# Kernel tuning notes

Hardware: AMD Instinct MI355X
Metric: run time of the kernel (lower is better)

Reference implementation:

```python
import jax, jax.numpy as jnp
import numpy as np

HEADS = 4
HEAD_DIM = 32
IN_DIM = 128
N_TRIG = 48
N_SPAN = 128


def build_edges(T, S):
    # nodes are (trig r, span c) flattened row-major: n = r*S + c
    N = T * S
    nodes = jnp.arange(N, dtype=jnp.int32)
    r = nodes // S
    c = nodes % S
    # same-row neighbors (includes self loop once): [N, S]
    row_nb = r[:, None] * S + jnp.arange(S, dtype=jnp.int32)[None, :]
    # same-column neighbors excluding own row: [N, T-1]
    t_idx = jnp.arange(T - 1, dtype=jnp.int32)[None, :]
    t = t_idx + (t_idx >= r[:, None]).astype(jnp.int32)
    col_nb = t * S + c[:, None]
    deg = S + T - 1
    src = jnp.concatenate([row_nb, col_nb], axis=1).reshape(-1)  # [N*deg]
    dst = jnp.repeat(nodes, deg)
    return src, dst, N


def gat_conv(x, src, dst, N, W, att_src, att_dst, bias):
    # PyG GATConv (eval mode, dropout off), concat=True.
    # W: [in, H*Hd]; att_src/att_dst: [H, Hd]; bias: [H*Hd]
    h = (x @ W).reshape(N, HEADS, HEAD_DIM)          # [N,H,Hd]
    a_src = jnp.sum(h * att_src[None], axis=-1)      # [N,H]
    a_dst = jnp.sum(h * att_dst[None], axis=-1)      # [N,H]
    e = jax.nn.leaky_relu(a_src[src] + a_dst[dst], negative_slope=0.2)  # [E,H]
    # scatter-softmax over incoming edges per destination node
    m = jax.ops.segment_max(e, dst, num_segments=N)  # [N,H]
    ex = jnp.exp(e - m[dst])
    denom = jax.ops.segment_sum(ex, dst, num_segments=N)
    alpha = ex / denom[dst]                          # [E,H]
    msg = alpha[:, :, None] * h[src]                 # [E,H,Hd]
    out = jax.ops.segment_sum(msg, dst, num_segments=N)  # [N,H,Hd]
    return out.reshape(N, HEADS * HEAD_DIM) + bias[None]


def setup_inputs() -> dict:
    key = jax.random.key(0)
    ks = jax.random.split(key, 9)
    D = IN_DIM
    HD = HEADS * HEAD_DIM
    inp = {
        "pair_embeddings": jax.random.normal(ks[0], (1, N_TRIG, N_SPAN, D), dtype=jnp.float32),
        "W1": jax.random.normal(ks[1], (D, HD), dtype=jnp.float32) * (2.0 / (D + HD)) ** 0.5,
        "att_src1": jax.random.normal(ks[2], (HEADS, HEAD_DIM), dtype=jnp.float32) * 0.1,
        "att_dst1": jax.random.normal(ks[3], (HEADS, HEAD_DIM), dtype=jnp.float32) * 0.1,
        "b1": jnp.zeros((HD,), dtype=jnp.float32),
        "W2": jax.random.normal(ks[4], (HD, HD), dtype=jnp.float32) * (2.0 / (HD + HD)) ** 0.5,
        "att_src2": jax.random.normal(ks[5], (HEADS, HEAD_DIM), dtype=jnp.float32) * 0.1,
        "att_dst2": jax.random.normal(ks[6], (HEADS, HEAD_DIM), dtype=jnp.float32) * 0.1,
        "b2": jnp.zeros((HD,), dtype=jnp.float32),
        "num_trigs_kept": N_TRIG,
        "num_arg_spans_kept": N_SPAN,
    }
    return inp


def reference(pair_embeddings, W1, att_src1, att_dst1, b1, W2, att_src2, att_dst2, b2, num_trigs_kept, num_arg_spans_kept):
    T, S = int(num_trigs_kept), int(num_arg_spans_kept)
    src, dst, N = build_edges(T, S)
    # batch_size == 1: slice and flatten node features
    x = pair_embeddings[0, :T, :S].reshape(N, -1)
    x = jax.nn.elu(gat_conv(x, src, dst, N, W1, att_src1, att_dst1, b1))
    x = jax.nn.elu(gat_conv(x, src, dst, N, W2, att_src2, att_dst2, b2))
    return x
```

## Files before the change

kernel.cpp:

```cpp
#include <hip/hip_runtime.h>

#define T_TRIG 48
#define S_SPAN 128
#define NN (T_TRIG * S_SPAN)
#define D 128

typedef __attribute__((ext_vector_type(8))) short sh8;
typedef __attribute__((ext_vector_type(4))) float f32x4;

__device__ inline unsigned short f2bf(float v) {
    unsigned u = __float_as_uint(v);
    unsigned r = u + 0x7FFFu + ((u >> 16) & 1u);
    return (unsigned short)(r >> 16);
}
__device__ inline float bf2f(unsigned short b) {
    return __uint_as_float(((unsigned)b) << 16);
}

__global__ __launch_bounds__(64) void pack_w_kernel(
    const float* __restrict__ W1, const float* __restrict__ W2,
    unsigned short* __restrict__ w1h, unsigned short* __restrict__ w1l,
    unsigned short* __restrict__ w2h, unsigned short* __restrict__ w2l)
{
    const int b = blockIdx.x;
    const int l = threadIdx.x;
    const float* W = (b < 8) ? W1 : W2;
    unsigned short* wh = (b < 8) ? w1h : w2h;
    unsigned short* wl = (b < 8) ? w1l : w2l;
    const int nt = b & 7;
    const int n = nt * 16 + (l & 15);
    const int kgb = (l >> 4) * 8;

    #pragma unroll
    for (int kc = 0; kc < 4; ++kc) {
        unsigned short hb[8], lb[8];
        #pragma unroll
        for (int i = 0; i < 8; ++i) {
            int k = kc * 32 + kgb + i;
            float v = W[k * D + n];
            unsigned short h = f2bf(v);
            hb[i] = h;
            lb[i] = f2bf(v - bf2f(h));
        }
        size_t base = ((size_t)(nt * 4 + kc) * 64 + l) * 8;
        #pragma unroll
        for (int i = 0; i < 8; ++i) { wh[base + i] = hb[i]; wl[base + i] = lb[i]; }
    }
}

__global__ __launch_bounds__(64) void gemm_mfma_kernel(
    const float* __restrict__ X,
    const unsigned short* __restrict__ Wh, const unsigned short* __restrict__ Wl,
    const float* __restrict__ att_s, const float* __restrict__ att_d,
    float* __restrict__ H, float* __restrict__ asrc, float* __restrict__ adst)
{
    const int l = threadIdx.x;
    const int mt = blockIdx.x >> 1;
    const int nh = blockIdx.x & 1;
    const int c = l & 15;
    const int kg = l >> 4;
    const int row0 = mt * 16;

    const sh8* Wh8 = (const sh8*)Wh;
    const sh8* Wl8 = (const sh8*)Wl;

    f32x4 acc[4] = {f32x4{0,0,0,0}, f32x4{0,0,0,0}, f32x4{0,0,0,0}, f32x4{0,0,0,0}};

    #pragma unroll
    for (int kc = 0; kc < 4; ++kc) {
        const float* xp = X + (size_t)(row0 + c) * D + kc * 32 + kg * 8;
        float4 x0 = *(const float4*)xp;
        float4 x1 = *(const float4*)(xp + 4);
        float xs[8] = {x0.x, x0.y, x0.z, x0.w, x1.x, x1.y, x1.z, x1.w};
        sh8 ah, al;
        #pragma unroll
        for (int i = 0; i < 8; ++i) {
            unsigned short h = f2bf(xs[i]);
            ah[i] = (short)h;
            al[i] = (short)f2bf(xs[i] - bf2f(h));
        }
        #pragma unroll
        for (int ntl = 0; ntl < 4; ++ntl) {
            int ntg = nh * 4 + ntl;
            sh8 bh = Wh8[(ntg * 4 + kc) * 64 + l];
            sh8 bl = Wl8[(ntg * 4 + kc) * 64 + l];
            acc[ntl] = __builtin_amdgcn_mfma_f32_16x16x32_bf16(ah, bh, acc[ntl], 0, 0, 0);
            acc[ntl] = __builtin_amdgcn_mfma_f32_16x16x32_bf16(al, bh, acc[ntl], 0, 0, 0);
            acc[ntl] = __builtin_amdgcn_mfma_f32_16x16x32_bf16(ah, bl, acc[ntl], 0, 0, 0);
        }
    }

    #pragma unroll
    for (int ntl = 0; ntl < 4; ++ntl) {
        #pragma unroll
        for (int i = 0; i < 4; ++i) {
            H[(size_t)(row0 + kg * 4 + i) * D + nh * 64 + ntl * 16 + c] = acc[ntl][i];
        }
    }

    float asv[4], adv[4];
    #pragma unroll
    for (int ntl = 0; ntl < 4; ++ntl) {
        int d = (nh * 2 + (ntl >> 1)) * 32 + (ntl & 1) * 16 + c;
        asv[ntl] = att_s[d];
        adv[ntl] = att_d[d];
    }
    #pragma unroll
    for (int i = 0; i < 4; ++i) {
        float ps0 = acc[0][i] * asv[0] + acc[1][i] * asv[1];
        float ps1 = acc[2][i] * asv[2] + acc[3][i] * asv[3];
        float pd0 = acc[0][i] * adv[0] + acc[1][i] * adv[1];
        float pd1 = acc[2][i] * adv[2] + acc[3][i] * adv[3];
        #pragma unroll
        for (int o = 1; o < 16; o <<= 1) {
            ps0 += __shfl_xor(ps0, o); ps1 += __shfl_xor(ps1, o);
            pd0 += __shfl_xor(pd0, o); pd1 += __shfl_xor(pd1, o);
        }
        if (c == 0) {
            int rr = row0 + kg * 4 + i;
            asrc[rr * 4 + nh * 2 + 0] = ps0;
            asrc[rr * 4 + nh * 2 + 1] = ps1;
            adst[rr * 4 + nh * 2 + 0] = pd0;
            adst[rr * 4 + nh * 2 + 1] = pd1;
        }
    }
}

__global__ __launch_bounds__(256) void row_agg_kernel(
    const float* __restrict__ H, const float* __restrict__ asrc,
    const float* __restrict__ adst, float* __restrict__ num_row,
    float* __restrict__ den_row)
{
    __shared__ float sh_h[S_SPAN][32];
    __shared__ float sh_as[S_SPAN];
    const int tid = threadIdx.x;
    const int r = blockIdx.x >> 2;
    const int h = blockIdx.x & 3;
    const int base = r * S_SPAN;

    #pragma unroll
    for (int it = 0; it < 4; ++it) {
        int chunk = tid + it * 256;
        int cp = chunk >> 3, fc = chunk & 7;
        *(float4*)&sh_h[cp][fc * 4] =
            *(const float4*)&H[(size_t)(base + cp) * D + h * 32 + fc * 4];
    }
    if (tid < S_SPAN) sh_as[tid] = asrc[(base + tid) * 4 + h];
    __syncthreads();

    const int fg = tid & 3;
    const int cth = tid >> 2;
    const float ad0 = adst[(base + cth) * 4 + h];
    const float ad1 = adst[(base + cth + 64) * 4 + h];
    float4 n00 = {0,0,0,0}, n01 = {0,0,0,0}, n10 = {0,0,0,0}, n11 = {0,0,0,0};
    float den0 = 0.f, den1 = 0.f;

    #pragma unroll 2
    for (int cp = 0; cp < S_SPAN; ++cp) {
        float a = sh_as[cp];
        float4 h0 = *(float4*)&sh_h[cp][fg * 8];
        float4 h1 = *(float4*)&sh_h[cp][fg * 8 + 4];
        float e0 = a + ad0; e0 = fmaxf(e0, 0.2f * e0);
        float e1 = a + ad1; e1 = fmaxf(e1, 0.2f * e1);
        float w0 = __expf(e0);
        float w1 = __expf(e1);
        den0 += w0; den1 += w1;
        n00.x = fmaf(w0, h0.x, n00.x); n00.y = fmaf(w0, h0.y, n00.y);
        n00.z = fmaf(w0, h0.z, n00.z); n00.w = fmaf(w0, h0.w, n00.w);
        n01.x = fmaf(w0, h1.x, n01.x); n01.y = fmaf(w0, h1.y, n01.y);
        n01.z = fmaf(w0, h1.z, n01.z); n01.w = fmaf(w0, h1.w, n01.w);
        n10.x = fmaf(w1, h0.x, n10.x); n10.y = fmaf(w1, h0.y, n10.y);
        n10.z = fmaf(w1, h0.z, n10.z); n10.w = fmaf(w1, h0.w, n10.w);
        n11.x = fmaf(w1, h1.x, n11.x); n11.y = fmaf(w1, h1.y, n11.y);
        n11.z = fmaf(w1, h1.z, n11.z); n11.w = fmaf(w1, h1.w, n11.w);
    }

    const int n0 = base + cth, n1 = n0 + 64;
    *(float4*)&num_row[(size_t)n0 * D + h * 32 + fg * 8]     = n00;
    *(float4*)&num_row[(size_t)n0 * D + h * 32 + fg * 8 + 4] = n01;
    *(float4*)&num_row[(size_t)n1 * D + h * 32 + fg * 8]     = n10;
    *(float4*)&num_row[(size_t)n1 * D + h * 32 + fg * 8 + 4] = n11;
    if (fg == 0) {
        den_row[n0 * 4 + h] = den0;
        den_row[n1 * 4 + h] = den1;
    }
}

__global__ __launch_bounds__(256) void col_agg_kernel(
    const float* __restrict__ H, const float* __restrict__ asrc,
    const float* __restrict__ adst, const float* __restrict__ num_row,
    const float* __restrict__ den_row, const float* __restrict__ bias,
    float* __restrict__ out)
{
    __shared__ float sh_h[T_TRIG][D];
    __shared__ float sh_as[4][T_TRIG];
    const int c = blockIdx.x;
    const int tid = threadIdx.x;

    #pragma unroll
    for (int it = 0; it < 6; ++it) {
        int chunk = tid + it * 256;
        int t = chunk >> 5, fc = chunk & 31;
        *(float4*)&sh_h[t][fc * 4] =
            *(const float4*)&H[(size_t)(t * S_SPAN + c) * D + fc * 4];
    }
    if (tid < 4 * T_TRIG) {
        int hh = tid / T_TRIG, t = tid - hh * T_TRIG;
        sh_as[hh][t] = asrc[(t * S_SPAN + c) * 4 + hh];
    }
    __syncthreads();

    const int f4g = tid & 31;
    const int tg = tid >> 5;
    const int head = f4g >> 3;

    float4 num[6];
    float den[6], ad[6];
    #pragma unroll
    for (int dd = 0; dd < 6; ++dd) {
        num[dd] = {0,0,0,0};
        den[dd] = 0.f;
        ad[dd] = adst[((tg * 6 + dd) * S_SPAN + c) * 4 + head];
    }

    for (int tp = 0; tp < T_TRIG; ++tp) {
        float a = sh_as[head][tp];
        float4 hv = *(float4*)&sh_h[tp][f4g * 4];
        #pragma unroll
        for (int dd = 0; dd < 6; ++dd) {
            float e = a + ad[dd];
            e = fmaxf(e, 0.2f * e);
            float w = __expf(e);
            w = (tp == tg * 6 + dd) ? 0.f : w;
            den[dd] += w;
            num[dd].x = fmaf(w, hv.x, num[dd].x);
            num[dd].y = fmaf(w, hv.y, num[dd].y);
            num[dd].z = fmaf(w, hv.z, num[dd].z);
            num[dd].w = fmaf(w, hv.w, num[dd].w);
        }
    }

    const float4 b4 = *(const float4*)&bias[f4g * 4];
    #pragma unroll
    for (int dd = 0; dd < 6; ++dd) {
        int n = (tg * 6 + dd) * S_SPAN + c;
        float4 nr = *(const float4*)&num_row[(size_t)n * D + f4g * 4];
        float dr = den_row[n * 4 + head];
        float inv = 1.f / (dr + den[dd]);
        float4 o;
        o.x = (nr.x + num[dd].x) * inv + b4.x;
        o.y = (nr.y + num[dd].y) * inv + b4.y;
        o.z = (nr.z + num[dd].z) * inv + b4.z;
        o.w = (nr.w + num[dd].w) * inv + b4.w;
        o.x = o.x > 0.f ? o.x : (__expf(o.x) - 1.f);
        o.y = o.y > 0.f ? o.y : (__expf(o.y) - 1.f);
        o.z = o.z > 0.f ? o.z : (__expf(o.z) - 1.f);
        o.w = o.w > 0.f ? o.w : (__expf(o.w) - 1.f);
        *(float4*)&out[(size_t)n * D + f4g * 4] = o;
    }
}

extern "C" void kernel_launch(void* const* d_in, const int* in_sizes, int n_in,
                              void* d_out, int out_size, void* d_ws, size_t ws_size,
                              hipStream_t stream)
{
    const float* pe  = (const float*)d_in[0];
    const float* W1  = (const float*)d_in[1];
    const float* as1 = (const float*)d_in[2];
    const float* ad1 = (const float*)d_in[3];
    const float* b1  = (const float*)d_in[4];
    const float* W2  = (const float*)d_in[5];
    const float* as2 = (const float*)d_in[6];
    const float* ad2 = (const float*)d_in[7];
    const float* b2  = (const float*)d_in[8];
    float* out = (float*)d_out;

    char* ws = (char*)d_ws;
    float* H     = (float*)ws;
    float* X2    = H + (size_t)NN * D;
    float* numr  = X2 + (size_t)NN * D;
    float* asrcb = numr + (size_t)NN * D;
    float* adstb = asrcb + (size_t)NN * 4;
    float* denb  = adstb + (size_t)NN * 4;
    unsigned short* w1h = (unsigned short*)(denb + (size_t)NN * 4);
    unsigned short* w1l = w1h + 128 * 128;
    unsigned short* w2h = w1l + 128 * 128;
    unsigned short* w2l = w2h + 128 * 128;

    pack_w_kernel<<<dim3(16), dim3(64), 0, stream>>>(W1, W2, w1h, w1l, w2h, w2l);

    gemm_mfma_kernel<<<dim3(768), dim3(64), 0, stream>>>(pe, w1h, w1l, as1, ad1, H, asrcb, adstb);
    row_agg_kernel<<<dim3(T_TRIG * 4), dim3(256), 0, stream>>>(H, asrcb, adstb, numr, denb);
    col_agg_kernel<<<dim3(S_SPAN), dim3(256), 0, stream>>>(H, asrcb, adstb, numr, denb, b1, X2);
    gemm_mfma_kernel<<<dim3(768), dim3(64), 0, stream>>>(X2, w2h, w2l, as2, ad2, H, asrcb, adstb);
    row_agg_kernel<<<dim3(T_TRIG * 4), dim3(256), 0, stream>>>(H, asrcb, adstb, numr, denb);
    col_agg_kernel<<<dim3(S_SPAN), dim3(256), 0, stream>>>(H, asrcb, adstb, numr, denb, b2, out);
}
```

Measured before the change: 78.42 us.

## Pre-split activations into bf16 hi/lo and widen GEMM to 4 waves per block

Input activations are now converted to bf16 hi/lo pairs once, in a prep kernel for layer 1 and in the col_agg epilogue for layer 2, so the GEMM loads pre-packed operands instead of converting fp32 per block. The GEMM block grows to 256 threads, with each wave owning one 16-column tile, and the attention-score reduction is finished through shared memory. The weight packing is folded into the same prep launch. The split format writes and reads two bf16 buffers in place of one fp32 buffer, and the prep pass adds extra traffic over the layer-1 input.

Result: slower. 81.57 us (+4.0%).

```diff
diff --git a/kernel.cpp b/kernel.cpp
--- a/kernel.cpp
+++ b/kernel.cpp
@@ -7,6 +7,7 @@
 
 typedef __attribute__((ext_vector_type(8))) short sh8;
 typedef __attribute__((ext_vector_type(4))) float f32x4;
+typedef __attribute__((ext_vector_type(4))) unsigned short us4;
 
 __device__ inline unsigned short f2bf(float v) {
     unsigned u = __float_as_uint(v);
@@ -17,27 +18,28 @@
     return __uint_as_float(((unsigned)b) << 16);
 }
 
-__global__ __launch_bounds__(64) void pack_w_kernel(
-    const float* __restrict__ W1, const float* __restrict__ W2,
+__global__ __launch_bounds__(256) void prep_kernel(
+    const float* __restrict__ pe, const float* __restrict__ W1,
+    const float* __restrict__ W2,
+    unsigned short* __restrict__ x1h, unsigned short* __restrict__ x1l,
     unsigned short* __restrict__ w1h, unsigned short* __restrict__ w1l,
     unsigned short* __restrict__ w2h, unsigned short* __restrict__ w2l)
 {
     const int b = blockIdx.x;
-    const int l = threadIdx.x;
-    const float* W = (b < 8) ? W1 : W2;
-    unsigned short* wh = (b < 8) ? w1h : w2h;
-    unsigned short* wl = (b < 8) ? w1l : w2l;
-    const int nt = b & 7;
-    const int n = nt * 16 + (l & 15);
-    const int kgb = (l >> 4) * 8;
-
-    #pragma unroll
-    for (int kc = 0; kc < 4; ++kc) {
+    const int t = threadIdx.x;
+    if (b < 16) {
+        const float* W = (b < 8) ? W1 : W2;
+        unsigned short* wh = (b < 8) ? w1h : w2h;
+        unsigned short* wl = (b < 8) ? w1l : w2l;
+        const int nt = b & 7;
+        const int kc = t >> 6;
+        const int l = t & 63;
+        const int n = nt * 16 + (l & 15);
+        const int kb = kc * 32 + (l >> 4) * 8;
         unsigned short hb[8], lb[8];
         #pragma unroll
         for (int i = 0; i < 8; ++i) {
-            int k = kc * 32 + kgb + i;
-            float v = W[k * D + n];
+            float v = W[(kb + i) * D + n];
             unsigned short h = f2bf(v);
             hb[i] = h;
             lb[i] = f2bf(v - bf2f(h));
@@ -45,84 +47,87 @@
         size_t base = ((size_t)(nt * 4 + kc) * 64 + l) * 8;
         #pragma unroll
         for (int i = 0; i < 8; ++i) { wh[base + i] = hb[i]; wl[base + i] = lb[i]; }
-    }
-}
-
-__global__ __launch_bounds__(64) void gemm_mfma_kernel(
-    const float* __restrict__ X,
+    } else {
+        const int idx = (b - 16) * 256 + t;
+        const float* p = pe + (size_t)idx * 8;
+        float4 v0 = *(const float4*)p;
+        float4 v1 = *(const float4*)(p + 4);
+        float xs[8] = {v0.x, v0.y, v0.z, v0.w, v1.x, v1.y, v1.z, v1.w};
+        sh8 hv, lv;
+        #pragma unroll
+        for (int i = 0; i < 8; ++i) {
+            unsigned short h = f2bf(xs[i]);
+            hv[i] = (short)h;
+            lv[i] = (short)f2bf(xs[i] - bf2f(h));
+        }
+        ((sh8*)x1h)[idx] = hv;
+        ((sh8*)x1l)[idx] = lv;
+    }
+}
+
+__global__ __launch_bounds__(256) void gemm_mfma_kernel(
+    const unsigned short* __restrict__ Xh, const unsigned short* __restrict__ Xl,
     const unsigned short* __restrict__ Wh, const unsigned short* __restrict__ Wl,
     const float* __restrict__ att_s, const float* __restrict__ att_d,
     float* __restrict__ H, float* __restrict__ asrc, float* __restrict__ adst)
 {
-    const int l = threadIdx.x;
+    __shared__ float ps_part[4][16], pd_part[4][16];
+
+    const int t = threadIdx.x;
+    const int w = t >> 6;
+    const int l = t & 63;
     const int mt = blockIdx.x >> 1;
-    const int nh = blockIdx.x & 1;
+    const int nq = blockIdx.x & 1;
+    const int nt = nq * 4 + w;
     const int c = l & 15;
     const int kg = l >> 4;
     const int row0 = mt * 16;
 
+    const sh8* Xh8 = (const sh8*)Xh;
+    const sh8* Xl8 = (const sh8*)Xl;
     const sh8* Wh8 = (const sh8*)Wh;
     const sh8* Wl8 = (const sh8*)Wl;
 
-    f32x4 acc[4] = {f32x4{0,0,0,0}, f32x4{0,0,0,0}, f32x4{0,0,0,0}, f32x4{0,0,0,0}};
-
+    f32x4 acc = {0, 0, 0, 0};
     #pragma unroll
     for (int kc = 0; kc < 4; ++kc) {
-        const float* xp = X + (size_t)(row0 + c) * D + kc * 32 + kg * 8;
-        float4 x0 = *(const float4*)xp;
-        float4 x1 = *(const float4*)(xp + 4);
-        float xs[8] = {x0.x, x0.y, x0.z, x0.w, x1.x, x1.y, x1.z, x1.w};
-        sh8 ah, al;
-        #pragma unroll
-        for (int i = 0; i < 8; ++i) {
-            unsigned short h = f2bf(xs[i]);
-            ah[i] = (short)h;
-            al[i] = (short)f2bf(xs[i] - bf2f(h));
-        }
-        #pragma unroll
-        for (int ntl = 0; ntl < 4; ++ntl) {
-            int ntg = nh * 4 + ntl;
-            sh8 bh = Wh8[(ntg * 4 + kc) * 64 + l];
-            sh8 bl = Wl8[(ntg * 4 + kc) * 64 + l];
-            acc[ntl] = __builtin_amdgcn_mfma_f32_16x16x32_bf16(ah, bh, acc[ntl], 0, 0, 0);
-            acc[ntl] = __builtin_amdgcn_mfma_f32_16x16x32_bf16(al, bh, acc[ntl], 0, 0, 0);
-            acc[ntl] = __builtin_amdgcn_mfma_f32_16x16x32_bf16(ah, bl, acc[ntl], 0, 0, 0);
-        }
-    }
-
-    #pragma unroll
-    for (int ntl = 0; ntl < 4; ++ntl) {
-        #pragma unroll
-        for (int i = 0; i < 4; ++i) {
-            H[(size_t)(row0 + kg * 4 + i) * D + nh * 64 + ntl * 16 + c] = acc[ntl][i];
-        }
-    }
-
-    float asv[4], adv[4];
-    #pragma unroll
-    for (int ntl = 0; ntl < 4; ++ntl) {
-        int d = (nh * 2 + (ntl >> 1)) * 32 + (ntl & 1) * 16 + c;
-        asv[ntl] = att_s[d];
-        adv[ntl] = att_d[d];
-    }
+        const int xi = (row0 + c) * 16 + kc * 4 + kg;
+        sh8 ah = Xh8[xi];
+        sh8 al = Xl8[xi];
+        sh8 bh = Wh8[(nt * 4 + kc) * 64 + l];
+        sh8 bl = Wl8[(nt * 4 + kc) * 64 + l];
+        acc = __builtin_amdgcn_mfma_f32_16x16x32_bf16(ah, bh, acc, 0, 0, 0);
+        acc = __builtin_amdgcn_mfma_f32_16x16x32_bf16(al, bh, acc, 0, 0, 0);
+        acc = __builtin_amdgcn_mfma_f32_16x16x32_bf16(ah, bl, acc, 0, 0, 0);
+    }
+
+    #pragma unroll
+    for (int i = 0; i < 4; ++i)
+        H[(size_t)(row0 + kg * 4 + i) * D + nt * 16 + c] = acc[i];
+
+    const int dim = (nt >> 1) * 32 + (nt & 1) * 16 + c;
+    const float asv = att_s[dim];
+    const float adv = att_d[dim];
     #pragma unroll
     for (int i = 0; i < 4; ++i) {
-        float ps0 = acc[0][i] * asv[0] + acc[1][i] * asv[1];
-        float ps1 = acc[2][i] * asv[2] + acc[3][i] * asv[3];
-        float pd0 = acc[0][i] * adv[0] + acc[1][i] * adv[1];
-        float pd1 = acc[2][i] * adv[2] + acc[3][i] * adv[3];
-        #pragma unroll
-        for (int o = 1; o < 16; o <<= 1) {
-            ps0 += __shfl_xor(ps0, o); ps1 += __shfl_xor(ps1, o);
-            pd0 += __shfl_xor(pd0, o); pd1 += __shfl_xor(pd1, o);
-        }
+        float ps = acc[i] * asv;
+        float pd = acc[i] * adv;
+        ps += __shfl_xor(ps, 1); pd += __shfl_xor(pd, 1);
+        ps += __shfl_xor(ps, 2); pd += __shfl_xor(pd, 2);
+        ps += __shfl_xor(ps, 4); pd += __shfl_xor(pd, 4);
+        ps += __shfl_xor(ps, 8); pd += __shfl_xor(pd, 8);
         if (c == 0) {
-            int rr = row0 + kg * 4 + i;
-            asrc[rr * 4 + nh * 2 + 0] = ps0;
-            asrc[rr * 4 + nh * 2 + 1] = ps1;
-            adst[rr * 4 + nh * 2 + 0] = pd0;
-            adst[rr * 4 + nh * 2 + 1] = pd1;
-        }
+            ps_part[w][kg * 4 + i] = ps;
+            pd_part[w][kg * 4 + i] = pd;
+        }
+    }
+    __syncthreads();
+    if (t < 32) {
+        const int row = t & 15;
+        const int hh = t >> 4;
+        const int head = nq * 2 + hh;
+        asrc[(row0 + row) * 4 + head] = ps_part[2 * hh][row] + ps_part[2 * hh + 1][row];
+        adst[(row0 + row) * 4 + head] = pd_part[2 * hh][row] + pd_part[2 * hh + 1][row];
     }
 }
 
@@ -190,7 +195,8 @@
     const float* __restrict__ H, const float* __restrict__ asrc,
     const float* __restrict__ adst, const float* __restrict__ num_row,
     const float* __restrict__ den_row, const float* __restrict__ bias,
-    float* __restrict__ out)
+    float* __restrict__ out, unsigned short* __restrict__ xh,
+    unsigned short* __restrict__ xl)
 {
     __shared__ float sh_h[T_TRIG][D];
     __shared__ float sh_as[4][T_TRIG];
@@ -247,16 +253,28 @@
         float4 nr = *(const float4*)&num_row[(size_t)n * D + f4g * 4];
         float dr = den_row[n * 4 + head];
         float inv = 1.f / (dr + den[dd]);
-        float4 o;
-        o.x = (nr.x + num[dd].x) * inv + b4.x;
-        o.y = (nr.y + num[dd].y) * inv + b4.y;
-        o.z = (nr.z + num[dd].z) * inv + b4.z;
-        o.w = (nr.w + num[dd].w) * inv + b4.w;
-        o.x = o.x > 0.f ? o.x : (__expf(o.x) - 1.f);
-        o.y = o.y > 0.f ? o.y : (__expf(o.y) - 1.f);
-        o.z = o.z > 0.f ? o.z : (__expf(o.z) - 1.f);
-        o.w = o.w > 0.f ? o.w : (__expf(o.w) - 1.f);
-        *(float4*)&out[(size_t)n * D + f4g * 4] = o;
+        float o[4];
+        o[0] = (nr.x + num[dd].x) * inv + b4.x;
+        o[1] = (nr.y + num[dd].y) * inv + b4.y;
+        o[2] = (nr.z + num[dd].z) * inv + b4.z;
+        o[3] = (nr.w + num[dd].w) * inv + b4.w;
+        #pragma unroll
+        for (int q = 0; q < 4; ++q)
+            o[q] = o[q] > 0.f ? o[q] : (__expf(o[q]) - 1.f);
+        if (xh) {
+            us4 hv4, lv4;
+            #pragma unroll
+            for (int q = 0; q < 4; ++q) {
+                unsigned short hq = f2bf(o[q]);
+                hv4[q] = hq;
+                lv4[q] = f2bf(o[q] - bf2f(hq));
+            }
+            *(us4*)&xh[(size_t)n * D + f4g * 4] = hv4;
+            *(us4*)&xl[(size_t)n * D + f4g * 4] = lv4;
+        } else {
+            float4 o4 = {o[0], o[1], o[2], o[3]};
+            *(float4*)&out[(size_t)n * D + f4g * 4] = o4;
+        }
     }
 }
 
@@ -277,22 +295,30 @@
 
     char* ws = (char*)d_ws;
     float* H     = (float*)ws;
-    float* X2    = H + (size_t)NN * D;
-    float* numr  = X2 + (size_t)NN * D;
+    float* numr  = H + (size_t)NN * D;
     float* asrcb = numr + (size_t)NN * D;
     float* adstb = asrcb + (size_t)NN * 4;
     float* denb  = adstb + (size_t)NN * 4;
-    unsigned short* w1h = (unsigned short*)(denb + (size_t)NN * 4);
-    unsigned short* w1l = w1h + 128 * 128;
-    unsigned short* w2h = w1l + 128 * 128;
-    unsigned short* w2l = w2h + 128 * 128;
-
-    pack_w_kernel<<<dim3(16), dim3(64), 0, stream>>>(W1, W2, w1h, w1l, w2h, w2l);
-
-    gemm_mfma_kernel<<<dim3(768), dim3(64), 0, stream>>>(pe, w1h, w1l, as1, ad1, H, asrcb, adstb);
+    unsigned short* x1h = (unsigned short*)(denb + (size_t)NN * 4);
+    unsigned short* x1l = x1h + (size_t)NN * D;
+    unsigned short* x2h = x1l + (size_t)NN * D;
+    unsigned short* x2l = x2h + (size_t)NN * D;
+    unsigned short* w1h = x2l + (size_t)NN * D;
+    unsigned short* w1l = w1h + D * D;
+    unsigned short* w2h = w1l + D * D;
+    unsigned short* w2l = w2h + D * D;
+
+    prep_kernel<<<dim3(16 + NN * D / 8 / 256), dim3(256), 0, stream>>>(
+        pe, W1, W2, x1h, x1l, w1h, w1l, w2h, w2l);
+
+    gemm_mfma_kernel<<<dim3(NN / 16 * 2), dim3(256), 0, stream>>>(
+        x1h, x1l, w1h, w1l, as1, ad1, H, asrcb, adstb);
     row_agg_kernel<<<dim3(T_TRIG * 4), dim3(256), 0, stream>>>(H, asrcb, adstb, numr, denb);
-    col_agg_kernel<<<dim3(S_SPAN), dim3(256), 0, stream>>>(H, asrcb, adstb, numr, denb, b1, X2);
-    gemm_mfma_kernel<<<dim3(768), dim3(64), 0, stream>>>(X2, w2h, w2l, as2, ad2, H, asrcb, adstb);
+    col_agg_kernel<<<dim3(S_SPAN), dim3(256), 0, stream>>>(
+        H, asrcb, adstb, numr, denb, b1, nullptr, x2h, x2l);
+    gemm_mfma_kernel<<<dim3(NN / 16 * 2), dim3(256), 0, stream>>>(
+        x2h, x2l, w2h, w2l, as2, ad2, H, asrcb, adstb);
     row_agg_kernel<<<dim3(T_TRIG * 4), dim3(256), 0, stream>>>(H, asrcb, adstb, numr, denb);
-    col_agg_kernel<<<dim3(S_SPAN), dim3(256), 0, stream>>>(H, asrcb, adstb, numr, denb, b2, out);
-}
+    col_agg_kernel<<<dim3(S_SPAN), dim3(256), 0, stream>>>(
+        H, asrcb, adstb, numr, denb, b2, out, nullptr, nullptr);
+}
```
